# Kernel optimization log

Measured on AMD Instinct MI355X. Metric: run time of the kernel, lower is better.

The kernel has to match this reference:

```python
import jax, jax.numpy as jnp
import numpy as np

B, C_IN, C, H, W = 32, 2048, 1024, 14, 14
N_CLS = 30


def setup_inputs() -> dict:
    key = jax.random.key(0)
    k1, k2, k3, k4, k5 = jax.random.split(key, 5)
    f1 = jax.random.normal(k1, (B, C_IN, H, W), dtype=jnp.float32)
    f2 = jax.random.normal(k2, (B, C, H, W), dtype=jnp.float32)
    conv_w = jax.random.normal(k3, (C, C_IN), dtype=jnp.float32) * (1.0 / np.sqrt(C_IN))
    fc_w = jax.random.normal(k4, (N_CLS, C), dtype=jnp.float32) * (1.0 / np.sqrt(C))
    fc_b = jax.random.normal(k5, (N_CLS,), dtype=jnp.float32)
    return {"f1": f1, "f2": f2, "conv_w": conv_w, "fc_w": fc_w, "fc_b": fc_b}


def reference(f1, f2, conv_w, fc_w, fc_b):
    # conv1: 1x1 conv 2048 -> 1024, no bias  => channel contraction
    f1c = jnp.einsum('bihw,oi->bohw', f1, conv_w)  # [B, C, H, W]

    # bilinear_pooling: out[b,c,h,i,j] = f1c[b,c,h,i] * f2[b,c,h,j]
    # followed by AdaptiveAvgPool2d((1,1)) over (H, W*W).
    # mean_{h,i,j} f1c*f2 = mean_h[ (mean_i f1c) * (mean_j f2) ]
    xm = jnp.mean(f1c, axis=-1)              # [B, C, H]
    ym = jnp.mean(f2, axis=-1)               # [B, C, H]
    pooled = jnp.mean(xm * ym, axis=-1)      # [B, C]

    # fc head
    return pooled @ fc_w.T + fc_b            # [B, 30]
```

## Files before the change

kernel.cpp:

```cpp
#include <hip/hip_runtime.h>
#include <hip/hip_bf16.h>


typedef __attribute__((ext_vector_type(8))) short short8;
typedef __attribute__((ext_vector_type(4))) float f32x4;

static __device__ __forceinline__ unsigned short f2bf(float f) {
    union { float f; unsigned u; } v; v.f = f;
    return (unsigned short)((v.u + 0x7FFFu + ((v.u >> 16) & 1u)) >> 16);
}

#define LROW 197

__global__ __launch_bounds__(256) void k1_prep(
    const float* __restrict__ f1, const float* __restrict__ f2,
    const float* __restrict__ cw,
    unsigned short* __restrict__ f1mt, unsigned short* __restrict__ cwb,
    float* __restrict__ ym)
{
    __shared__ float lds[64 * LROW];
    const float inv14 = 1.0f / 14.0f;
    int blk = blockIdx.x;
    int tid = threadIdx.x;

    if (blk < 1024) {
        int b = blk >> 5, i0 = (blk & 31) * 64;
        const float4* src = (const float4*)(f1 + (size_t)(b * 2048 + i0) * 196);
        #pragma unroll
        for (int j = 0; j < 13; j++) {
            unsigned idx = j * 256 + tid;
            if (idx < 3136) {
                unsigned row = idx / 49, col = idx - row * 49;
                *(float4*)&lds[row * LROW + col * 4] = src[idx];
            }
        }
        __syncthreads();
        int r  = tid & 63;
        int hb = tid >> 6;
        unsigned short* o = f1mt + (size_t)b * 16 * 2048 + i0 + r;
        #pragma unroll
        for (int it = 0; it < 4; it++) {
            int h = hb + it * 4;
            if (h < 14) {
                const float* p = &lds[r * LROW + h * 14];
                float s = 0.0f;
                #pragma unroll
                for (int q = 0; q < 14; q++) s += p[q];
                o[h * 2048] = f2bf(s * inv14);
            } else {
                o[h * 2048] = 0;
            }
        }
    } else if (blk < 1536) {
        int t = blk - 1024;
        int b = t >> 4, c0 = (t & 15) * 64;
        const float4* src = (const float4*)(f2 + (size_t)(b * 1024 + c0) * 196);
        #pragma unroll
        for (int j = 0; j < 13; j++) {
            unsigned idx = j * 256 + tid;
            if (idx < 3136) {
                unsigned row = idx / 49, col = idx - row * 49;
                *(float4*)&lds[row * LROW + col * 4] = src[idx];
            }
        }
        __syncthreads();
        int r  = tid & 63;
        int hb = tid >> 6;
        float* o = ym + (size_t)b * 16 * 1024 + c0 + r;
        #pragma unroll
        for (int it = 0; it < 4; it++) {
            int h = hb + it * 4;
            if (h < 14) {
                const float* p = &lds[r * LROW + h * 14];
                float s = 0.0f;
                #pragma unroll
                for (int q = 0; q < 14; q++) s += p[q];
                o[h * 1024] = s * inv14;
            } else {
                o[h * 1024] = 0.0f;
            }
        }
    } else {
        int t = (blk - 1536) * 256 + tid;
        const float4* p = (const float4*)(cw + (size_t)t * 8);
        float4 v0 = p[0], v1 = p[1];
        ushort4 a, b4;
        a.x = f2bf(v0.x); a.y = f2bf(v0.y); a.z = f2bf(v0.z); a.w = f2bf(v0.w);
        b4.x = f2bf(v1.x); b4.y = f2bf(v1.y); b4.z = f2bf(v1.z); b4.w = f2bf(v1.w);
        *(ushort4*)(cwb + (size_t)t * 8)     = a;
        *(ushort4*)(cwb + (size_t)t * 8 + 4) = b4;
    }
}

__global__ __launch_bounds__(256) void k2_gemm(
    const unsigned short* __restrict__ A,
    const unsigned short* __restrict__ Bm,
    const float* __restrict__ ym,
    float* __restrict__ part)
{
    int tid = threadIdx.x;
    int w  = tid >> 6;
    int l  = tid & 63;
    int lg = l >> 4;
    int lr = l & 15;

    int bid = blockIdx.x;
    int sid = (bid & 7) * 128 + (bid >> 3);
    int ct  = sid >> 6;
    int rem = sid & 63;
    int nt  = rem >> 2;
    int kq  = rem & 3;
    int c0 = ct * 64, n0 = nt * 32;
    int kc = kq * 4 + w;
    int kbase = kc * 128;

    const unsigned short* Ap = A  + (size_t)(c0 + lr) * 2048 + kbase + lg * 8;
    const unsigned short* Bp = Bm + (size_t)(n0 + lr) * 2048 + kbase + lg * 8;

    f32x4 acc[4][2];
    #pragma unroll
    for (int mf = 0; mf < 4; mf++)
        #pragma unroll
        for (int nf = 0; nf < 2; nf++)
            acc[mf][nf] = (f32x4){0.f, 0.f, 0.f, 0.f};

    #pragma unroll 1
    for (int half = 0; half < 2; half++) {
        short8 af[4][2], bf[2][2];
        #pragma unroll
        for (int kk = 0; kk < 2; kk++) {
            int ko = half * 64 + kk * 32;
            #pragma unroll
            for (int mf = 0; mf < 4; mf++)
                af[mf][kk] = *(const short8*)(Ap + mf * 16 * 2048 + ko);
            #pragma unroll
            for (int nf = 0; nf < 2; nf++)
                bf[nf][kk] = *(const short8*)(Bp + nf * 16 * 2048 + ko);
        }
        #pragma unroll
        for (int kk = 0; kk < 2; kk++)
            #pragma unroll
            for (int mf = 0; mf < 4; mf++)
                #pragma unroll
                for (int nf = 0; nf < 2; nf++)
                    acc[mf][nf] = __builtin_amdgcn_mfma_f32_16x16x32_bf16(
                        af[mf][kk], bf[nf][kk], acc[mf][nf], 0, 0, 0);
    }

    const float inv14 = 1.0f / 14.0f;
    #pragma unroll
    for (int nf = 0; nf < 2; nf++) {
        int b = nt * 2 + nf;
        const float* yrow = ym + (size_t)(b * 16 + lr) * 1024 + c0 + lg * 4;
        #pragma unroll
        for (int mf = 0; mf < 4; mf++) {
            f32x4 yv = *(const f32x4*)(yrow + mf * 16);
            f32x4 pp = acc[mf][nf] * yv;
            #pragma unroll
            for (int st = 1; st <= 8; st <<= 1) {
                pp[0] += __shfl_xor(pp[0], st);
                pp[1] += __shfl_xor(pp[1], st);
                pp[2] += __shfl_xor(pp[2], st);
                pp[3] += __shfl_xor(pp[3], st);
            }
            if (lr == 0) {
                float* dst = part + (size_t)kc * 32768 + b * 1024 + c0 + mf * 16 + lg * 4;
                *(f32x4*)dst = pp * inv14;
            }
        }
    }
}

__global__ __launch_bounds__(1024) void k3_fc(
    const float* __restrict__ part, const float* __restrict__ fcw,
    const float* __restrict__ fcb, float* __restrict__ out)
{
    __shared__ float ps[1024];
    int b = blockIdx.x, tid = threadIdx.x;
    float s = 0.0f;
    #pragma unroll
    for (int k = 0; k < 16; k++)
        s += part[(size_t)k * 32768 + b * 1024 + tid];
    ps[tid] = s;
    __syncthreads();
    int w = tid >> 6, l = tid & 63;
    for (int n = w; n < 30; n += 16) {
        const float* wp = fcw + n * 1024;
        float t = 0.0f;
        #pragma unroll
        for (int it = 0; it < 16; it++)
            t += wp[l + it * 64] * ps[l + it * 64];
        #pragma unroll
        for (int m = 32; m; m >>= 1) t += __shfl_xor(t, m);
        if (l == 0) out[b * 30 + n] = t + fcb[n];
    }
}

extern "C" void kernel_launch(void* const* d_in, const int* in_sizes, int n_in,
                              void* d_out, int out_size, void* d_ws, size_t ws_size,
                              hipStream_t stream) {
    const float* f1  = (const float*)d_in[0];
    const float* f2  = (const float*)d_in[1];
    const float* cw  = (const float*)d_in[2];
    const float* fcw = (const float*)d_in[3];
    const float* fcb = (const float*)d_in[4];
    float* out = (float*)d_out;

    unsigned short* f1mt = (unsigned short*)d_ws;
    unsigned short* cwb  = (unsigned short*)((char*)d_ws + (2u << 20));
    float* ym            = (float*)((char*)d_ws + (6u << 20));
    float* part          = (float*)((char*)d_ws + (8u << 20));

    k1_prep<<<2560, 256, 0, stream>>>(f1, f2, cw, f1mt, cwb, ym);
    k2_gemm<<<1024, 256, 0, stream>>>(cwb, f1mt, ym, part);
    k3_fc<<<32, 1024, 0, stream>>>(part, fcw, fcb, out);
}
```

Measured before the change: 133.9 us.

## Pre-pack GEMM operands into MFMA fragment order for coalesced loads

The prep kernel now writes conv weights, the pooled f1 means and the f2 means directly in the per-lane fragment order the MFMA loop consumes. Each wavefront's short8 load then reads one contiguous 1 KB chunk instead of 16 strided rows. The prep work is split into smaller 32-channel blocks, so it launches more of them and adds an extra LDS transpose stage. This aims to cut uncoalesced global traffic in the GEMM, at the cost of slightly more complex and scattered writes during prep.

```diff
diff --git a/kernel.cpp b/kernel.cpp
--- a/kernel.cpp
+++ b/kernel.cpp
@@ -10,92 +10,104 @@
     return (unsigned short)((v.u + 0x7FFFu + ((v.u >> 16) & 1u)) >> 16);
 }
 
-#define LROW 197
+#define JA 2048
+#define JB (JA + 1024)
+#define JC (JB + 1024)
 
 __global__ __launch_bounds__(256) void k1_prep(
     const float* __restrict__ f1, const float* __restrict__ f2,
     const float* __restrict__ cw,
-    unsigned short* __restrict__ f1mt, unsigned short* __restrict__ cwb,
-    float* __restrict__ ym)
+    unsigned short* __restrict__ afrag, unsigned short* __restrict__ bfrag,
+    float* __restrict__ ymf)
 {
-    __shared__ float lds[64 * LROW];
+    __shared__ float lds[32 * 196];
+    __shared__ float s_lds[32 * 16];
     const float inv14 = 1.0f / 14.0f;
-    int blk = blockIdx.x;
-    int tid = threadIdx.x;
-
-    if (blk < 1024) {
-        int b = blk >> 5, i0 = (blk & 31) * 64;
+    int blk = blockIdx.x, tid = threadIdx.x;
+
+    if (blk < JA) {
+        int b = blk >> 6, kk = blk & 63;
+        int i0 = kk * 32;
         const float4* src = (const float4*)(f1 + (size_t)(b * 2048 + i0) * 196);
         #pragma unroll
-        for (int j = 0; j < 13; j++) {
-            unsigned idx = j * 256 + tid;
-            if (idx < 3136) {
-                unsigned row = idx / 49, col = idx - row * 49;
-                *(float4*)&lds[row * LROW + col * 4] = src[idx];
-            }
-        }
-        __syncthreads();
-        int r  = tid & 63;
-        int hb = tid >> 6;
-        unsigned short* o = f1mt + (size_t)b * 16 * 2048 + i0 + r;
-        #pragma unroll
-        for (int it = 0; it < 4; it++) {
-            int h = hb + it * 4;
+        for (int j = 0; j < 7; j++) {
+            int idx = j * 256 + tid;
+            if (idx < 1568) *(float4*)&lds[idx * 4] = src[idx];
+        }
+        __syncthreads();
+        #pragma unroll
+        for (int it = 0; it < 2; it++) {
+            int r = tid & 31, h = (tid >> 5) + it * 8;
+            float s = 0.0f;
             if (h < 14) {
-                const float* p = &lds[r * LROW + h * 14];
-                float s = 0.0f;
+                const float* p = &lds[r * 196 + h * 14];
                 #pragma unroll
                 for (int q = 0; q < 14; q++) s += p[q];
-                o[h * 2048] = f2bf(s * inv14);
-            } else {
-                o[h * 2048] = 0;
-            }
-        }
-    } else if (blk < 1536) {
-        int t = blk - 1024;
-        int b = t >> 4, c0 = (t & 15) * 64;
+                s *= inv14;
+            }
+            s_lds[r * 16 + h] = s;
+        }
+        __syncthreads();
+        if (tid < 64) {
+            int lr = tid & 15, lg = tid >> 4;
+            short8 pk;
+            #pragma unroll
+            for (int j = 0; j < 8; j++)
+                pk[j] = (short)f2bf(s_lds[(lg * 8 + j) * 16 + lr]);
+            *(short8*)(bfrag + (((size_t)b * 64 + kk) * 64 + tid) * 8) = pk;
+        }
+    } else if (blk < JB) {
+        int t = blk - JA;
+        int b = t >> 5, cc = t & 31;
+        int c0 = cc * 32;
         const float4* src = (const float4*)(f2 + (size_t)(b * 1024 + c0) * 196);
         #pragma unroll
-        for (int j = 0; j < 13; j++) {
-            unsigned idx = j * 256 + tid;
-            if (idx < 3136) {
-                unsigned row = idx / 49, col = idx - row * 49;
-                *(float4*)&lds[row * LROW + col * 4] = src[idx];
-            }
-        }
-        __syncthreads();
-        int r  = tid & 63;
-        int hb = tid >> 6;
-        float* o = ym + (size_t)b * 16 * 1024 + c0 + r;
-        #pragma unroll
-        for (int it = 0; it < 4; it++) {
-            int h = hb + it * 4;
+        for (int j = 0; j < 7; j++) {
+            int idx = j * 256 + tid;
+            if (idx < 1568) *(float4*)&lds[idx * 4] = src[idx];
+        }
+        __syncthreads();
+        #pragma unroll
+        for (int it = 0; it < 2; it++) {
+            int r = tid & 31, h = (tid >> 5) + it * 8;
+            float s = 0.0f;
             if (h < 14) {
-                const float* p = &lds[r * LROW + h * 14];
-                float s = 0.0f;
+                const float* p = &lds[r * 196 + h * 14];
                 #pragma unroll
                 for (int q = 0; q < 14; q++) s += p[q];
-                o[h * 1024] = s * inv14;
-            } else {
-                o[h * 1024] = 0.0f;
-            }
+                s *= inv14;
+            }
+            s_lds[r * 16 + h] = s;
+        }
+        __syncthreads();
+        if (tid < 128) {
+            int cql = tid >> 4, h = tid & 15;
+            f32x4 v;
+            #pragma unroll
+            for (int e = 0; e < 4; e++)
+                v[e] = s_lds[(cql * 4 + e) * 16 + h];
+            *(f32x4*)(ymf + (((size_t)b * 256 + cc * 8 + cql) * 16 + h) * 4) = v;
         }
     } else {
-        int t = (blk - 1536) * 256 + tid;
-        const float4* p = (const float4*)(cw + (size_t)t * 8);
+        int t = (blk - JB) * 256 + tid;
+        int l = t & 63, kkg = (t >> 6) & 63, c_blk = t >> 12;
+        int c  = c_blk * 16 + (l & 15);
+        int i0 = kkg * 32 + (l >> 4) * 8;
+        const float4* p = (const float4*)(cw + (size_t)c * 2048 + i0);
         float4 v0 = p[0], v1 = p[1];
-        ushort4 a, b4;
-        a.x = f2bf(v0.x); a.y = f2bf(v0.y); a.z = f2bf(v0.z); a.w = f2bf(v0.w);
-        b4.x = f2bf(v1.x); b4.y = f2bf(v1.y); b4.z = f2bf(v1.z); b4.w = f2bf(v1.w);
-        *(ushort4*)(cwb + (size_t)t * 8)     = a;
-        *(ushort4*)(cwb + (size_t)t * 8 + 4) = b4;
+        short8 pk;
+        pk[0] = (short)f2bf(v0.x); pk[1] = (short)f2bf(v0.y);
+        pk[2] = (short)f2bf(v0.z); pk[3] = (short)f2bf(v0.w);
+        pk[4] = (short)f2bf(v1.x); pk[5] = (short)f2bf(v1.y);
+        pk[6] = (short)f2bf(v1.z); pk[7] = (short)f2bf(v1.w);
+        *(short8*)(afrag + ((size_t)(c_blk * 64 + kkg) * 64 + l) * 8) = pk;
     }
 }
 
 __global__ __launch_bounds__(256) void k2_gemm(
-    const unsigned short* __restrict__ A,
-    const unsigned short* __restrict__ Bm,
-    const float* __restrict__ ym,
+    const unsigned short* __restrict__ afrag,
+    const unsigned short* __restrict__ bfrag,
+    const float* __restrict__ ymf,
     float* __restrict__ part)
 {
     int tid = threadIdx.x;
@@ -110,12 +122,8 @@
     int rem = sid & 63;
     int nt  = rem >> 2;
     int kq  = rem & 3;
-    int c0 = ct * 64, n0 = nt * 32;
+    int c0 = ct * 64;
     int kc = kq * 4 + w;
-    int kbase = kc * 128;
-
-    const unsigned short* Ap = A  + (size_t)(c0 + lr) * 2048 + kbase + lg * 8;
-    const unsigned short* Bp = Bm + (size_t)(n0 + lr) * 2048 + kbase + lg * 8;
 
     f32x4 acc[4][2];
     #pragma unroll
@@ -128,33 +136,35 @@
     for (int half = 0; half < 2; half++) {
         short8 af[4][2], bf[2][2];
         #pragma unroll
-        for (int kk = 0; kk < 2; kk++) {
-            int ko = half * 64 + kk * 32;
+        for (int kkh = 0; kkh < 2; kkh++) {
+            int kkg = kc * 4 + half * 2 + kkh;
             #pragma unroll
             for (int mf = 0; mf < 4; mf++)
-                af[mf][kk] = *(const short8*)(Ap + mf * 16 * 2048 + ko);
+                af[mf][kkh] = *(const short8*)(
+                    afrag + ((size_t)((ct * 4 + mf) * 64 + kkg) * 64 + l) * 8);
             #pragma unroll
             for (int nf = 0; nf < 2; nf++)
-                bf[nf][kk] = *(const short8*)(Bp + nf * 16 * 2048 + ko);
-        }
-        #pragma unroll
-        for (int kk = 0; kk < 2; kk++)
+                bf[nf][kkh] = *(const short8*)(
+                    bfrag + ((size_t)((nt * 2 + nf) * 64 + kkg) * 64 + l) * 8);
+        }
+        #pragma unroll
+        for (int kkh = 0; kkh < 2; kkh++)
             #pragma unroll
             for (int mf = 0; mf < 4; mf++)
                 #pragma unroll
                 for (int nf = 0; nf < 2; nf++)
                     acc[mf][nf] = __builtin_amdgcn_mfma_f32_16x16x32_bf16(
-                        af[mf][kk], bf[nf][kk], acc[mf][nf], 0, 0, 0);
+                        af[mf][kkh], bf[nf][kkh], acc[mf][nf], 0, 0, 0);
     }
 
     const float inv14 = 1.0f / 14.0f;
     #pragma unroll
     for (int nf = 0; nf < 2; nf++) {
         int b = nt * 2 + nf;
-        const float* yrow = ym + (size_t)(b * 16 + lr) * 1024 + c0 + lg * 4;
         #pragma unroll
         for (int mf = 0; mf < 4; mf++) {
-            f32x4 yv = *(const f32x4*)(yrow + mf * 16);
+            f32x4 yv = *(const f32x4*)(
+                ymf + (((size_t)b * 256 + ct * 16 + mf * 4 + lg) * 16 + lr) * 4);
             f32x4 pp = acc[mf][nf] * yv;
             #pragma unroll
             for (int st = 1; st <= 8; st <<= 1) {
@@ -206,12 +216,12 @@
     const float* fcb = (const float*)d_in[4];
     float* out = (float*)d_out;
 
-    unsigned short* f1mt = (unsigned short*)d_ws;
-    unsigned short* cwb  = (unsigned short*)((char*)d_ws + (2u << 20));
-    float* ym            = (float*)((char*)d_ws + (6u << 20));
-    float* part          = (float*)((char*)d_ws + (8u << 20));
-
-    k1_prep<<<2560, 256, 0, stream>>>(f1, f2, cw, f1mt, cwb, ym);
-    k2_gemm<<<1024, 256, 0, stream>>>(cwb, f1mt, ym, part);
+    unsigned short* afrag = (unsigned short*)d_ws;
+    unsigned short* bfrag = (unsigned short*)((char*)d_ws + (4u << 20));
+    float* ymf            = (float*)((char*)d_ws + (6u << 20));
+    float* part           = (float*)((char*)d_ws + (8u << 20));
+
+    k1_prep<<<4096, 256, 0, stream>>>(f1, f2, cw, afrag, bfrag, ymf);
+    k2_gemm<<<1024, 256, 0, stream>>>(afrag, bfrag, ymf, part);
     k3_fc<<<32, 1024, 0, stream>>>(part, fcw, fcb, out);
 }
```

New measurement: 127.1 us. -5.1%, faster.
